# Kernel tuning notes

Hardware: AMD Instinct MI355X
Metric: run time of the kernel (lower is better)

The kernel has to match this reference:

```python
import jax, jax.numpy as jnp
import numpy as np

B, SQ, SK, DQ, DKV, DH, DV = 8, 2048, 2048, 1024, 1024, 1024, 1024


def setup_inputs() -> dict:
    ks = jax.random.split(jax.random.key(0), 10)
    q = jax.random.normal(ks[0], (B, SQ, DQ), dtype=jnp.float32)
    k = jax.random.normal(ks[1], (B, SK, DKV), dtype=jnp.float32)
    v = jax.random.normal(ks[2], (B, SK, DKV), dtype=jnp.float32)
    mask = jax.random.randint(ks[3], (B, SK), 0, 2).astype(jnp.bool_)
    s = 1.0 / np.sqrt(DQ)
    Wq = jax.random.normal(ks[4], (DQ, DH), dtype=jnp.float32) * s
    bq = jnp.zeros((DH,), dtype=jnp.float32)
    Wk = jax.random.normal(ks[5], (DKV, DH), dtype=jnp.float32) * s
    bk = jnp.zeros((DH,), dtype=jnp.float32)
    Wv = jax.random.normal(ks[6], (DKV, DV), dtype=jnp.float32) * s
    bv = jnp.zeros((DV,), dtype=jnp.float32)
    return {"q": q, "k": k, "v": v, "mask": mask,
            "Wq": Wq, "bq": bq, "Wk": Wk, "bk": bk, "Wv": Wv, "bv": bv}


def reference(q, k, v, mask, Wq, bq, Wk, bk, Wv, bv):
    # Linear projections
    Qp = q @ Wq + bq                       # [B, SQ, DH]
    Kp = k @ Wk + bk                       # [B, SK, DH]
    Vp = jnp.tanh(v @ Wv + bv)             # [B, SK, DV] (value has Tanh)
    # Scores; NOTE: original adds the *bool* mask, i.e. +0/+1, not -inf masking
    qk = jnp.einsum('bqd,bkd->bqk', Qp, Kp)
    qk = qk + mask[:, None, :].astype(qk.dtype)   # broadcast of mask.unsqueeze(1)
    attn = jax.nn.softmax(qk, axis=-1)
    out = jnp.einsum('bqk,bkd->bqd', attn, Vp)    # [B, SQ, DV]
    return out
```

## Files before the change

kernel.cpp:

```cpp
#include <hip/hip_runtime.h>
#include <math.h>

#define BB 8
#define SQL 2048
#define SKL 2048
#define DD 1024

typedef __attribute__((ext_vector_type(8))) short bf16x8;
typedef __attribute__((ext_vector_type(4))) float f32x4;
typedef __attribute__((ext_vector_type(4))) unsigned short us4;
typedef unsigned short u16;

__device__ __forceinline__ u16 f2bf(float f) {
    unsigned u = __float_as_uint(f);
    u += 0x7fffu + ((u >> 16) & 1u);
    return (u16)(u >> 16);
}
__device__ __forceinline__ float bf2f(u16 h) {
    return __uint_as_float((unsigned)h << 16);
}

__global__ __launch_bounds__(256)
void split3(const float* __restrict__ in, u16* __restrict__ oh,
            u16* __restrict__ ol, long n4) {
    long i = (long)blockIdx.x * 256 + threadIdx.x;
    if (i >= n4) return;
    float4 v = ((const float4*)in)[i];
    us4 h, l;
    h.x = f2bf(v.x); l.x = f2bf(v.x - bf2f(h.x));
    h.y = f2bf(v.y); l.y = f2bf(v.y - bf2f(h.y));
    h.z = f2bf(v.z); l.z = f2bf(v.z - bf2f(h.z));
    h.w = f2bf(v.w); l.w = f2bf(v.w - bf2f(h.w));
    ((us4*)oh)[i] = h;
    ((us4*)ol)[i] = l;
}

__global__ __launch_bounds__(256)
void splitT3(const float* __restrict__ W, u16* __restrict__ WhT,
             u16* __restrict__ WlT) {
    __shared__ float t[32][33];
    const int n0 = blockIdx.x * 32, k0 = blockIdx.y * 32;
    const int tx = threadIdx.x & 31, ty = threadIdx.x >> 5;
#pragma unroll
    for (int r = 0; r < 32; r += 8)
        t[ty + r][tx] = W[(long)(k0 + ty + r) * DD + n0 + tx];
    __syncthreads();
#pragma unroll
    for (int r = 0; r < 32; r += 8) {
        float x = t[tx][ty + r];
        u16 h = f2bf(x);
        WhT[(long)(n0 + ty + r) * DD + k0 + tx] = h;
        WlT[(long)(n0 + ty + r) * DD + k0 + tx] = f2bf(x - bf2f(h));
    }
}

#define GLL(gp, lp) __builtin_amdgcn_global_load_lds( \
    (const __attribute__((address_space(1))) void*)(gp), \
    (__attribute__((address_space(3))) void*)(lp), 16, 0, 0)

__global__ __launch_bounds__(512, 2)
void gemm3(const u16* __restrict__ Ah, const u16* __restrict__ Al,
           const u16* __restrict__ Bh, const u16* __restrict__ Bl,
           int lda, int ldb, int K, long sA, long sB,
           const float* __restrict__ bias, const int* __restrict__ mask, int sM,
           float* __restrict__ Cf, u16* __restrict__ C1, u16* __restrict__ C2,
           long sC, int ldc, int mode)
{
    __shared__ u16 L[65536];

    const int z = blockIdx.z;
    const long zA = (long)z * sA, zB = (long)z * sB;
    const int tid = threadIdx.x, lane = tid & 63, wave = tid >> 6;
    const int wm = wave >> 2, wn = wave & 3;
    const int l15 = lane & 15, lq = lane >> 4;
    const long row0 = (long)blockIdx.y * 256, col0 = (long)blockIdx.x * 256;

    const int pl = tid >> 8;
    const int c = tid & 255;
    const int srow = c >> 2;
    const int qg = (c & 3) ^ ((srow >> 1) & 3);
    const u16* sAp = (pl ? Al : Ah) + zA + qg * 8;
    const u16* sBp = (pl ? Bl : Bh) + zB + qg * 8;
    int ofA[4], ofB[4];
#pragma unroll
    for (int p = 0; p < 4; p++) {
        ofA[p] = (int)((row0 + p * 64 + srow) * (long)lda);
        ofB[p] = (int)((col0 + p * 64 + srow) * (long)ldb);
    }
    const int dst = tid * 8;

#define STB(p, kk, bb) GLL(sBp + ofB[p] + (kk), L + (bb) + 16384 + (p) * 4096 + dst)
#define STA(p, kk, bb) GLL(sAp + ofA[p] + (kk), L + (bb) + (p) * 4096 + dst)

    int aoff[8], boff[4];
#pragma unroll
    for (int i = 0; i < 8; i++) {
        int r = wm * 128 + i * 16 + l15;
        aoff[i] = (r >> 6) * 4096 + (r & 63) * 32 + ((lq ^ ((r >> 1) & 3)) * 8);
    }
#pragma unroll
    for (int j = 0; j < 4; j++) {
        int r = wn * 64 + j * 16 + l15;
        boff[j] = 16384 + (r >> 6) * 4096 + (r & 63) * 32 + ((lq ^ ((r >> 1) & 3)) * 8);
    }

    f32x4 acc[8][4];
#pragma unroll
    for (int i = 0; i < 8; i++)
#pragma unroll
        for (int j = 0; j < 4; j++)
#pragma unroll
            for (int e = 0; e < 4; e++) acc[i][j][e] = 0.f;

#define BAR() do { __builtin_amdgcn_s_barrier(); \
                   __builtin_amdgcn_sched_barrier(0); } while (0)

#define SPX(iA, iB, GLLCODE) do { \
    bf16x8 xh0 = *(const bf16x8*)(L + bo + aoff[iA]); \
    bf16x8 xl0 = *(const bf16x8*)(L + bo + aoff[iA] + 2048); \
    bf16x8 xh1 = *(const bf16x8*)(L + bo + aoff[iB]); \
    bf16x8 xl1 = *(const bf16x8*)(L + bo + aoff[iB] + 2048); \
    GLLCODE \
    __builtin_amdgcn_s_setprio(1); \
    _Pragma("unroll") \
    for (int j = 0; j < 4; j++) { \
        f32x4 t0 = acc[iA][j]; \
        t0 = __builtin_amdgcn_mfma_f32_16x16x32_bf16(xh0, yh[j], t0, 0, 0, 0); \
        t0 = __builtin_amdgcn_mfma_f32_16x16x32_bf16(xh0, yl[j], t0, 0, 0, 0); \
        t0 = __builtin_amdgcn_mfma_f32_16x16x32_bf16(xl0, yh[j], t0, 0, 0, 0); \
        acc[iA][j] = t0; \
        f32x4 t1 = acc[iB][j]; \
        t1 = __builtin_amdgcn_mfma_f32_16x16x32_bf16(xh1, yh[j], t1, 0, 0, 0); \
        t1 = __builtin_amdgcn_mfma_f32_16x16x32_bf16(xh1, yl[j], t1, 0, 0, 0); \
        t1 = __builtin_amdgcn_mfma_f32_16x16x32_bf16(xl1, yh[j], t1, 0, 0, 0); \
        acc[iB][j] = t1; \
    } \
    __builtin_amdgcn_s_setprio(0); \
} while (0)

#define TILEB(PF) do { \
    bf16x8 yh[4], yl[4]; \
    _Pragma("unroll") \
    for (int j = 0; j < 4; j++) { \
        yh[j] = *(const bf16x8*)(L + bo + boff[j]); \
        yl[j] = *(const bf16x8*)(L + bo + boff[j] + 2048); \
    } \
     \
    SPX(0, 1, if (PF) { STB(0, kn, bn); STB(1, kn, bn); }); \
    BAR(); \
     \
    SPX(2, 3, if (PF) { STB(2, kn, bn); STB(3, kn, bn); }); \
    if (PF) asm volatile("s_waitcnt vmcnt(4)" ::: "memory"); \
    else    asm volatile("s_waitcnt vmcnt(0)" ::: "memory"); \
    BAR(); \
     \
    SPX(4, 5, if (PF) { STA(0, kn, bn); STA(2, kn, bn); }); \
    BAR(); \
     \
    SPX(6, 7, if (PF) { STA(1, kn, bn); STA(3, kn, bn); }); \
    if (PF) { asm volatile("s_waitcnt vmcnt(2)" ::: "memory"); BAR(); } \
} while (0)

    const int NT = K >> 5;
    STB(0, 0, 0); STB(1, 0, 0); STB(2, 0, 0); STB(3, 0, 0);
    STA(0, 0, 0); STA(2, 0, 0); STA(1, 0, 0); STA(3, 0, 0);
    asm volatile("s_waitcnt vmcnt(2)" ::: "memory");
    BAR();

    for (int t = 0; t < NT - 1; ++t) {
        const int bo = (t & 1) << 15;
        const int bn = bo ^ 32768;
        const int kn = (t + 1) << 5;
        TILEB(1);
    }
    {
        const int bo = ((NT - 1) & 1) << 15;
        const int bn = bo ^ 32768; (void)bn;
        const int kn = 0; (void)kn;
        TILEB(0);
    }
#undef TILEB
#undef SPX
#undef BAR
#undef STA
#undef STB

    const long zc = (long)z * sC;
#pragma unroll
    for (int i = 0; i < 8; i++) {
#pragma unroll
        for (int j = 0; j < 4; j++) {
            const long col = col0 + wn * 64 + j * 16 + l15;
            const long rbase = row0 + wm * 128 + i * 16 + lq * 4;
            if (mode == 0 || mode == 3) {
                const float madd = (mode == 3) ? (float)mask[(long)z * sM + col] : 0.f;
#pragma unroll
                for (int r = 0; r < 4; r++)
                    Cf[zc + (rbase + r) * (long)ldc + col] = acc[i][j][r] + madd;
            } else if (mode == 1) {
                const float bv = bias[col];
#pragma unroll
                for (int r = 0; r < 4; r++) {
                    float val = acc[i][j][r] + bv;
                    u16 h = f2bf(val);
                    C1[zc + (rbase + r) * (long)ldc + col] = h;
                    C2[zc + (rbase + r) * (long)ldc + col] = f2bf(val - bf2f(h));
                }
            } else {
                const float bv = bias[col];
                us4 o;
                o.x = f2bf(tanhf(acc[i][j][0] + bv));
                o.y = f2bf(tanhf(acc[i][j][1] + bv));
                o.z = f2bf(tanhf(acc[i][j][2] + bv));
                o.w = f2bf(tanhf(acc[i][j][3] + bv));
                *(us4*)(C1 + zc + col * (long)ldc + rbase) = o;
            }
        }
    }
}

__global__ __launch_bounds__(256, 2)
void gemm1(const u16* __restrict__ A, const u16* __restrict__ B,
           float* __restrict__ C, int lda, int ldb, int K,
           long sA, long sB, long sC, int ldc)
{
    __shared__ u16 As[4096], Bs[4096];

    const int z = blockIdx.z;
    const long zA = (long)z * sA, zB = (long)z * sB;
    const int tid = threadIdx.x, lane = tid & 63, wave = tid >> 6;
    const int wm = (wave & 1) * 64, wn = (wave >> 1) * 64;
    const int l15 = lane & 15, lq = lane >> 4;
    const long row0 = (long)blockIdx.y * 128, col0 = (long)blockIdx.x * 128;

    long offA[2], offB[2]; int lds[2];
#pragma unroll
    for (int it = 0; it < 2; it++) {
        int c = tid + it * 256, row = c >> 2;
        int qg = (c & 3) ^ ((row >> 1) & 3);
        offA[it] = (row0 + row) * (long)lda + qg * 8;
        offB[it] = (col0 + row) * (long)ldb + qg * 8;
        lds[it] = c * 8;
    }
    int aoff[4], boff[4];
#pragma unroll
    for (int i = 0; i < 4; i++) {
        int r = wm + i * 16 + l15;
        aoff[i] = r * 32 + ((lq ^ ((r >> 1) & 3)) * 8);
    }
#pragma unroll
    for (int j = 0; j < 4; j++) {
        int r = wn + j * 16 + l15;
        boff[j] = r * 32 + ((lq ^ ((r >> 1) & 3)) * 8);
    }

    f32x4 acc[4][4];
#pragma unroll
    for (int i = 0; i < 4; i++)
#pragma unroll
        for (int j = 0; j < 4; j++)
#pragma unroll
            for (int e = 0; e < 4; e++) acc[i][j][e] = 0.f;

    for (int k0 = 0; k0 < K; k0 += 32) {
#pragma unroll
        for (int it = 0; it < 2; it++) {
            GLL(A + zA + offA[it] + k0, As + lds[it]);
            GLL(B + zB + offB[it] + k0, Bs + lds[it]);
        }
        __syncthreads();
        bf16x8 af[4], bf[4];
#pragma unroll
        for (int i = 0; i < 4; i++) af[i] = *(const bf16x8*)(As + aoff[i]);
#pragma unroll
        for (int j = 0; j < 4; j++) bf[j] = *(const bf16x8*)(Bs + boff[j]);
#pragma unroll
        for (int i = 0; i < 4; i++)
#pragma unroll
            for (int j = 0; j < 4; j++)
                acc[i][j] = __builtin_amdgcn_mfma_f32_16x16x32_bf16(af[i], bf[j], acc[i][j], 0, 0, 0);
        __syncthreads();
    }

    const long zc = (long)z * sC;
#pragma unroll
    for (int i = 0; i < 4; i++)
#pragma unroll
        for (int j = 0; j < 4; j++) {
            const long col = col0 + wn + j * 16 + l15;
            const long rbase = row0 + wm + i * 16 + lq * 4;
#pragma unroll
            for (int r = 0; r < 4; r++)
                C[zc + (rbase + r) * (long)ldc + col] = acc[i][j][r];
        }
}

__global__ __launch_bounds__(256)
void softmax_bf(float* __restrict__ S)
{
    float* p = S + (long)blockIdx.x * SKL;
    u16* po = (u16*)S + (long)blockIdx.x * 2 * SKL;
    const int tid = threadIdx.x;
    const int w = tid >> 6, lane = tid & 63;

    float4 v0 = *(float4*)(p + tid * 8);
    float4 v1 = *(float4*)(p + tid * 8 + 4);

    float m = fmaxf(fmaxf(fmaxf(v0.x, v0.y), fmaxf(v0.z, v0.w)),
                    fmaxf(fmaxf(v1.x, v1.y), fmaxf(v1.z, v1.w)));
#pragma unroll
    for (int off = 32; off; off >>= 1) m = fmaxf(m, __shfl_down(m, off));

    __shared__ float wm_[4], ws_[4];
    if (lane == 0) wm_[w] = m;
    __syncthreads();
    const float bm = fmaxf(fmaxf(wm_[0], wm_[1]), fmaxf(wm_[2], wm_[3]));

    v0.x = __expf(v0.x - bm); v0.y = __expf(v0.y - bm);
    v0.z = __expf(v0.z - bm); v0.w = __expf(v0.w - bm);
    v1.x = __expf(v1.x - bm); v1.y = __expf(v1.y - bm);
    v1.z = __expf(v1.z - bm); v1.w = __expf(v1.w - bm);

    float s = v0.x + v0.y + v0.z + v0.w + v1.x + v1.y + v1.z + v1.w;
#pragma unroll
    for (int off = 32; off; off >>= 1) s += __shfl_down(s, off);
    if (lane == 0) ws_[w] = s;
    __syncthreads();
    const float inv = 1.f / (ws_[0] + ws_[1] + ws_[2] + ws_[3]);

    us4 o0, o1;
    o0.x = f2bf(v0.x * inv); o0.y = f2bf(v0.y * inv);
    o0.z = f2bf(v0.z * inv); o0.w = f2bf(v0.w * inv);
    o1.x = f2bf(v1.x * inv); o1.y = f2bf(v1.y * inv);
    o1.z = f2bf(v1.z * inv); o1.w = f2bf(v1.w * inv);
    *(us4*)(po + tid * 8) = o0;
    *(us4*)(po + tid * 8 + 4) = o1;
}

extern "C" void kernel_launch(void* const* d_in, const int* in_sizes, int n_in,
                              void* d_out, int out_size, void* d_ws, size_t ws_size,
                              hipStream_t stream)
{
    const float* q  = (const float*)d_in[0];
    const float* k  = (const float*)d_in[1];
    const float* v  = (const float*)d_in[2];
    const int* mask = (const int*)d_in[3];
    const float* Wq = (const float*)d_in[4];
    const float* bq = (const float*)d_in[5];
    const float* Wk = (const float*)d_in[6];
    const float* bk = (const float*)d_in[7];
    const float* Wv = (const float*)d_in[8];
    const float* bv = (const float*)d_in[9];
    float* out = (float*)d_out;

    const long PZ = (long)SKL * DD;
    u16*   KpH = (u16*)d_ws;
    u16*   KpL = KpH + BB * PZ;
    u16*   Vt  = KpL + BB * PZ;
    float* S   = (float*)(Vt + BB * PZ);
    u16*   inH = (u16*)S;
    u16*   inL = inH + BB * PZ;
    u16*   WhT = inL + BB * PZ;
    u16*   WlT = WhT + (long)DD * DD;
    u16*   QpH = (u16*)d_out;
    u16*   QpL = QpH + BB * PZ;
    u16*   P   = (u16*)S;

    const dim3 b256(256), b512(512);
    const long n4 = BB * PZ / 4;
    const dim3 gSplit((unsigned)(n4 / 256));
    const dim3 gW(32, 32);
    const dim3 gProj(DD / 256, SQL / 256, BB);
    const dim3 gQK(SKL / 256, SQL / 256, BB);
    const dim3 gPV(8, 16, BB);
    const dim3 gSm(BB * SQL);

    split3<<<gSplit, b256, 0, stream>>>(q, inH, inL, n4);
    splitT3<<<gW, b256, 0, stream>>>(Wq, WhT, WlT);
    gemm3<<<gProj, b512, 0, stream>>>(inH, inL, WhT, WlT, DD, DD, DD, PZ, 0,
                                      bq, nullptr, 0, nullptr, QpH, QpL, PZ, DD, 1);
    split3<<<gSplit, b256, 0, stream>>>(k, inH, inL, n4);
    splitT3<<<gW, b256, 0, stream>>>(Wk, WhT, WlT);
    gemm3<<<gProj, b512, 0, stream>>>(inH, inL, WhT, WlT, DD, DD, DD, PZ, 0,
                                      bk, nullptr, 0, nullptr, KpH, KpL, PZ, DD, 1);
    split3<<<gSplit, b256, 0, stream>>>(v, inH, inL, n4);
    splitT3<<<gW, b256, 0, stream>>>(Wv, WhT, WlT);
    gemm3<<<gProj, b512, 0, stream>>>(inH, inL, WhT, WlT, DD, DD, DD, PZ, 0,
                                      bv, nullptr, 0, nullptr, Vt, nullptr, PZ, SKL, 2);
    gemm3<<<gQK, b512, 0, stream>>>(QpH, QpL, KpH, KpL, DD, DD, DD, PZ, PZ,
                                    nullptr, mask, SKL,
                                    S, nullptr, nullptr, (long)SQL * SKL, SKL, 3);
    softmax_bf<<<gSm, b256, 0, stream>>>(S);
    gemm1<<<gPV, b256, 0, stream>>>(P, Vt, out, 2 * SKL, SKL, SKL,
                                    (long)SQL * 2 * SKL, PZ,
                                    (long)SQL * DD, DD);
}
```

Before: 832.2 us.

## Rewrite PV GEMM with 256x256 double-buffered tiles and wave-per-row softmax

Replaces the simple 128x128 single-buffered PV GEMM with a 512-thread, 256x256-tile kernel. It double-buffers global-to-LDS loads so the next tile's prefetch overlaps the current MFMAs, and it uses setprio and split barriers. Softmax now handles one row per wave with xor shuffles, which removes the LDS reductions and block syncs. The larger tiles use more registers and LDS and produce fewer blocks, which may reduce occupancy.

```diff
diff --git a/kernel.cpp b/kernel.cpp
--- a/kernel.cpp
+++ b/kernel.cpp
@@ -181,7 +181,6 @@
     }
 #undef TILEB
 #undef SPX
-#undef BAR
 #undef STA
 #undef STB
 
@@ -217,124 +216,161 @@
             }
         }
     }
-}
-
-__global__ __launch_bounds__(256, 2)
-void gemm1(const u16* __restrict__ A, const u16* __restrict__ B,
-           float* __restrict__ C, int lda, int ldb, int K,
-           long sA, long sB, long sC, int ldc)
+#undef BAR
+}
+
+__global__ __launch_bounds__(512, 2)
+void gemm1w(const u16* __restrict__ A, const u16* __restrict__ B,
+            float* __restrict__ C, int lda, int ldb, int K,
+            long sA, long sB, long sC, int ldc)
 {
-    __shared__ u16 As[4096], Bs[4096];
+    __shared__ u16 L[32768];
 
     const int z = blockIdx.z;
     const long zA = (long)z * sA, zB = (long)z * sB;
     const int tid = threadIdx.x, lane = tid & 63, wave = tid >> 6;
-    const int wm = (wave & 1) * 64, wn = (wave >> 1) * 64;
+    const int wm = wave >> 2, wn = wave & 3;
     const int l15 = lane & 15, lq = lane >> 4;
-    const long row0 = (long)blockIdx.y * 128, col0 = (long)blockIdx.x * 128;
-
-    long offA[2], offB[2]; int lds[2];
-#pragma unroll
-    for (int it = 0; it < 2; it++) {
-        int c = tid + it * 256, row = c >> 2;
-        int qg = (c & 3) ^ ((row >> 1) & 3);
-        offA[it] = (row0 + row) * (long)lda + qg * 8;
-        offB[it] = (col0 + row) * (long)ldb + qg * 8;
-        lds[it] = c * 8;
-    }
-    int aoff[4], boff[4];
-#pragma unroll
-    for (int i = 0; i < 4; i++) {
-        int r = wm + i * 16 + l15;
+    const long row0 = (long)blockIdx.y * 256, col0 = (long)blockIdx.x * 256;
+
+    const int srow = tid >> 2;
+    const int qg = (tid & 3) ^ ((srow >> 1) & 3);
+    int ofA[2], ofB[2];
+#pragma unroll
+    for (int p = 0; p < 2; p++) {
+        ofA[p] = (int)((row0 + p * 128 + srow) * (long)lda) + qg * 8;
+        ofB[p] = (int)((col0 + p * 128 + srow) * (long)ldb) + qg * 8;
+    }
+    const int dst = tid * 8;
+
+#define STA1(p, kk, bb) GLL(A + zA + ofA[p] + (kk), L + (bb) + (p) * 4096 + dst)
+#define STB1(p, kk, bb) GLL(B + zB + ofB[p] + (kk), L + (bb) + 8192 + (p) * 4096 + dst)
+
+    int aoff[8], boff[4];
+#pragma unroll
+    for (int i = 0; i < 8; i++) {
+        int r = wm * 128 + i * 16 + l15;
         aoff[i] = r * 32 + ((lq ^ ((r >> 1) & 3)) * 8);
     }
 #pragma unroll
     for (int j = 0; j < 4; j++) {
-        int r = wn + j * 16 + l15;
-        boff[j] = r * 32 + ((lq ^ ((r >> 1) & 3)) * 8);
-    }
-
-    f32x4 acc[4][4];
-#pragma unroll
-    for (int i = 0; i < 4; i++)
+        int r = wn * 64 + j * 16 + l15;
+        boff[j] = 8192 + r * 32 + ((lq ^ ((r >> 1) & 3)) * 8);
+    }
+
+    f32x4 acc[8][4];
+#pragma unroll
+    for (int i = 0; i < 8; i++)
 #pragma unroll
         for (int j = 0; j < 4; j++)
 #pragma unroll
             for (int e = 0; e < 4; e++) acc[i][j][e] = 0.f;
 
-    for (int k0 = 0; k0 < K; k0 += 32) {
-#pragma unroll
-        for (int it = 0; it < 2; it++) {
-            GLL(A + zA + offA[it] + k0, As + lds[it]);
-            GLL(B + zB + offB[it] + k0, Bs + lds[it]);
-        }
-        __syncthreads();
-        bf16x8 af[4], bf[4];
-#pragma unroll
-        for (int i = 0; i < 4; i++) af[i] = *(const bf16x8*)(As + aoff[i]);
-#pragma unroll
-        for (int j = 0; j < 4; j++) bf[j] = *(const bf16x8*)(Bs + boff[j]);
-#pragma unroll
-        for (int i = 0; i < 4; i++)
-#pragma unroll
-            for (int j = 0; j < 4; j++)
-                acc[i][j] = __builtin_amdgcn_mfma_f32_16x16x32_bf16(af[i], bf[j], acc[i][j], 0, 0, 0);
-        __syncthreads();
-    }
+#define BAR() do { __builtin_amdgcn_s_barrier(); \
+                   __builtin_amdgcn_sched_barrier(0); } while (0)
+
+#define HALF1(i0) do { \
+    bf16x8 a0 = *(const bf16x8*)(L + bo + aoff[(i0) + 0]); \
+    bf16x8 a1 = *(const bf16x8*)(L + bo + aoff[(i0) + 1]); \
+    bf16x8 a2 = *(const bf16x8*)(L + bo + aoff[(i0) + 2]); \
+    bf16x8 a3 = *(const bf16x8*)(L + bo + aoff[(i0) + 3]); \
+    __builtin_amdgcn_s_setprio(1); \
+    _Pragma("unroll") \
+    for (int j = 0; j < 4; j++) { \
+        acc[(i0)+0][j] = __builtin_amdgcn_mfma_f32_16x16x32_bf16(a0, yh[j], acc[(i0)+0][j], 0, 0, 0); \
+        acc[(i0)+1][j] = __builtin_amdgcn_mfma_f32_16x16x32_bf16(a1, yh[j], acc[(i0)+1][j], 0, 0, 0); \
+        acc[(i0)+2][j] = __builtin_amdgcn_mfma_f32_16x16x32_bf16(a2, yh[j], acc[(i0)+2][j], 0, 0, 0); \
+        acc[(i0)+3][j] = __builtin_amdgcn_mfma_f32_16x16x32_bf16(a3, yh[j], acc[(i0)+3][j], 0, 0, 0); \
+    } \
+    __builtin_amdgcn_s_setprio(0); \
+} while (0)
+
+#define TILE1(PF) do { \
+    if (PF) { STB1(0, kn, bn); STB1(1, kn, bn); STA1(0, kn, bn); STA1(1, kn, bn); } \
+    __builtin_amdgcn_sched_barrier(0); \
+    bf16x8 yh[4]; \
+    _Pragma("unroll") \
+    for (int j = 0; j < 4; j++) yh[j] = *(const bf16x8*)(L + bo + boff[j]); \
+    HALF1(0); \
+    BAR(); \
+    HALF1(4); \
+    asm volatile("s_waitcnt vmcnt(0)" ::: "memory"); \
+    BAR(); \
+} while (0)
+
+    const int NT = K >> 5;
+    STB1(0, 0, 0); STB1(1, 0, 0); STA1(0, 0, 0); STA1(1, 0, 0);
+    asm volatile("s_waitcnt vmcnt(0)" ::: "memory");
+    BAR();
+
+    for (int t = 0; t < NT - 1; ++t) {
+        const int bo = (t & 1) << 14;
+        const int bn = bo ^ 16384;
+        const int kn = (t + 1) << 5;
+        TILE1(1);
+    }
+    {
+        const int bo = ((NT - 1) & 1) << 14;
+        const int bn = bo ^ 16384; (void)bn;
+        const int kn = 0; (void)kn;
+        TILE1(0);
+    }
+#undef TILE1
+#undef HALF1
+#undef BAR
+#undef STA1
+#undef STB1
 
     const long zc = (long)z * sC;
 #pragma unroll
-    for (int i = 0; i < 4; i++)
+    for (int i = 0; i < 8; i++)
 #pragma unroll
         for (int j = 0; j < 4; j++) {
-            const long col = col0 + wn + j * 16 + l15;
-            const long rbase = row0 + wm + i * 16 + lq * 4;
+            const long col = col0 + wn * 64 + j * 16 + l15;
+            const long rbase = row0 + wm * 128 + i * 16 + lq * 4;
 #pragma unroll
             for (int r = 0; r < 4; r++)
                 C[zc + (rbase + r) * (long)ldc + col] = acc[i][j][r];
         }
 }
 
-__global__ __launch_bounds__(256)
+__global__ __launch_bounds__(512)
 void softmax_bf(float* __restrict__ S)
 {
-    float* p = S + (long)blockIdx.x * SKL;
-    u16* po = (u16*)S + (long)blockIdx.x * 2 * SKL;
-    const int tid = threadIdx.x;
-    const int w = tid >> 6, lane = tid & 63;
-
-    float4 v0 = *(float4*)(p + tid * 8);
-    float4 v1 = *(float4*)(p + tid * 8 + 4);
-
-    float m = fmaxf(fmaxf(fmaxf(v0.x, v0.y), fmaxf(v0.z, v0.w)),
-                    fmaxf(fmaxf(v1.x, v1.y), fmaxf(v1.z, v1.w)));
-#pragma unroll
-    for (int off = 32; off; off >>= 1) m = fmaxf(m, __shfl_down(m, off));
-
-    __shared__ float wm_[4], ws_[4];
-    if (lane == 0) wm_[w] = m;
-    __syncthreads();
-    const float bm = fmaxf(fmaxf(wm_[0], wm_[1]), fmaxf(wm_[2], wm_[3]));
-
-    v0.x = __expf(v0.x - bm); v0.y = __expf(v0.y - bm);
-    v0.z = __expf(v0.z - bm); v0.w = __expf(v0.w - bm);
-    v1.x = __expf(v1.x - bm); v1.y = __expf(v1.y - bm);
-    v1.z = __expf(v1.z - bm); v1.w = __expf(v1.w - bm);
-
-    float s = v0.x + v0.y + v0.z + v0.w + v1.x + v1.y + v1.z + v1.w;
-#pragma unroll
-    for (int off = 32; off; off >>= 1) s += __shfl_down(s, off);
-    if (lane == 0) ws_[w] = s;
-    __syncthreads();
-    const float inv = 1.f / (ws_[0] + ws_[1] + ws_[2] + ws_[3]);
-
-    us4 o0, o1;
-    o0.x = f2bf(v0.x * inv); o0.y = f2bf(v0.y * inv);
-    o0.z = f2bf(v0.z * inv); o0.w = f2bf(v0.w * inv);
-    o1.x = f2bf(v1.x * inv); o1.y = f2bf(v1.y * inv);
-    o1.z = f2bf(v1.z * inv); o1.w = f2bf(v1.w * inv);
-    *(us4*)(po + tid * 8) = o0;
-    *(us4*)(po + tid * 8 + 4) = o1;
+    const long row = (long)blockIdx.x * 8 + (threadIdx.x >> 6);
+    float* p = S + row * SKL;
+    u16* po = (u16*)S + row * 2 * SKL;
+    const int lane = threadIdx.x & 63;
+
+    float4 v[8];
+#pragma unroll
+    for (int i = 0; i < 8; i++) v[i] = ((const float4*)p)[lane + 64 * i];
+
+    float m = -1e30f;
+#pragma unroll
+    for (int i = 0; i < 8; i++)
+        m = fmaxf(m, fmaxf(fmaxf(v[i].x, v[i].y), fmaxf(v[i].z, v[i].w)));
+#pragma unroll
+    for (int off = 32; off; off >>= 1) m = fmaxf(m, __shfl_xor(m, off));
+
+    float s = 0.f;
+#pragma unroll
+    for (int i = 0; i < 8; i++) {
+        v[i].x = __expf(v[i].x - m); v[i].y = __expf(v[i].y - m);
+        v[i].z = __expf(v[i].z - m); v[i].w = __expf(v[i].w - m);
+        s += v[i].x + v[i].y + v[i].z + v[i].w;
+    }
+#pragma unroll
+    for (int off = 32; off; off >>= 1) s += __shfl_xor(s, off);
+    const float inv = 1.f / s;
+
+#pragma unroll
+    for (int i = 0; i < 8; i++) {
+        us4 o;
+        o.x = f2bf(v[i].x * inv); o.y = f2bf(v[i].y * inv);
+        o.z = f2bf(v[i].z * inv); o.w = f2bf(v[i].w * inv);
+        ((us4*)po)[lane + 64 * i] = o;
+    }
 }
 
 extern "C" void kernel_launch(void* const* d_in, const int* in_sizes, int n_in,
@@ -372,8 +408,8 @@
     const dim3 gW(32, 32);
     const dim3 gProj(DD / 256, SQL / 256, BB);
     const dim3 gQK(SKL / 256, SQL / 256, BB);
-    const dim3 gPV(8, 16, BB);
-    const dim3 gSm(BB * SQL);
+    const dim3 gPV(DD / 256, SQL / 256, BB);
+    const dim3 gSm(BB * SQL / 8);
 
     split3<<<gSplit, b256, 0, stream>>>(q, inH, inL, n4);
     splitT3<<<gW, b256, 0, stream>>>(Wq, WhT, WlT);
@@ -390,8 +426,8 @@
     gemm3<<<gQK, b512, 0, stream>>>(QpH, QpL, KpH, KpL, DD, DD, DD, PZ, PZ,
                                     nullptr, mask, SKL,
                                     S, nullptr, nullptr, (long)SQL * SKL, SKL, 3);
-    softmax_bf<<<gSm, b256, 0, stream>>>(S);
-    gemm1<<<gPV, b256, 0, stream>>>(P, Vt, out, 2 * SKL, SKL, SKL,
-                                    (long)SQL * 2 * SKL, PZ,
-                                    (long)SQL * DD, DD);
-}
+    softmax_bf<<<gSm, b512, 0, stream>>>(S);
+    gemm1w<<<gPV, b512, 0, stream>>>(P, Vt, out, 2 * SKL, SKL, SKL,
+                                     (long)SQL * 2 * SKL, PZ,
+                                     (long)SQL * DD, DD);
+}
```

After: 812.2 us. 1.02x faster.
